# Optimization experiments

Hardware: AMD Instinct MI355X
Metric: run time of the kernel (lower is better)

The kernel has to match this reference:

```python
import jax, jax.numpy as jnp
import numpy as np

N, E, G = 10000, 160000, 64
F, C1, C2, C3, K, NC = 128, 128, 256, 512, 5, 10


def setup_inputs() -> dict:
    key = jax.random.key(0)
    ks = jax.random.split(key, 12)
    s = 0.05
    return {
        "x": jax.random.normal(ks[0], (N, F), dtype=jnp.float32),
        "edge_index": jax.random.randint(ks[1], (2, E), 0, N, dtype=jnp.int64),
        "batch": jnp.sort(jax.random.randint(ks[2], (N,), 0, G, dtype=jnp.int64)),
        "W_cheb": jax.random.normal(ks[3], (K, F, C1), dtype=jnp.float32) * s,
        "b_cheb": jnp.zeros((C1,), jnp.float32),
        "W_g1": jax.random.normal(ks[4], (C1, C2), dtype=jnp.float32) * s,
        "b_g1": jnp.zeros((C2,), jnp.float32),
        "W_g2": jax.random.normal(ks[5], (C2, C3), dtype=jnp.float32) * s,
        "b_g2": jnp.zeros((C3,), jnp.float32),
        "w_gate": jax.random.normal(ks[6], (C3, 1), dtype=jnp.float32) * s,
        "b_gate": jnp.zeros((1,), jnp.float32),
        "W_fc": jax.random.normal(ks[7], (C3, NC), dtype=jnp.float32) * s,
        "b_fc": jnp.zeros((NC,), jnp.float32),
    }


def _deg_inv_sqrt(deg):
    return jnp.where(deg > 0, jax.lax.rsqrt(jnp.maximum(deg, 1e-12)), 0.0)


def cheb_conv(x, src, dst, W, b):
    # PyG ChebConv, sym normalization, lambda_max=2 => scaled Laplacian = -D^-1/2 A D^-1/2
    ones = jnp.ones((src.shape[0],), x.dtype)
    deg = jax.ops.segment_sum(ones, src, num_segments=N)
    dinv = _deg_inv_sqrt(deg)
    w = -(dinv[src] * dinv[dst])  # [E]

    def prop(h):
        return jax.ops.segment_sum(w[:, None] * h[src], dst, num_segments=N)

    tx0 = x
    tx1 = prop(x)
    out = tx0 @ W[0] + tx1 @ W[1]
    for k in range(2, W.shape[0]):
        tx2 = 2.0 * prop(tx1) - tx0
        out = out + tx2 @ W[k]
        tx0, tx1 = tx1, tx2
    return out + b


def gcn_conv(x, src, dst, W, b):
    # PyG GCNConv: add self-loops, sym norm D~^-1/2 (A+I) D~^-1/2, transform then aggregate
    loop = jnp.arange(N, dtype=src.dtype)
    src_a = jnp.concatenate([src, loop])
    dst_a = jnp.concatenate([dst, loop])
    ones = jnp.ones((src_a.shape[0],), x.dtype)
    deg = jax.ops.segment_sum(ones, dst_a, num_segments=N)
    dinv = _deg_inv_sqrt(deg)
    norm = dinv[src_a] * dinv[dst_a]  # [E+N]
    h = x @ W
    return jax.ops.segment_sum(norm[:, None] * h[src_a], dst_a, num_segments=N) + b


def attention_pool(x, batch, w_gate, b_gate):
    logits = (x @ w_gate + b_gate)[:, 0]  # [N]
    m = jax.ops.segment_max(logits, batch, num_segments=G)
    e = jnp.exp(logits - m[batch])
    s = jax.ops.segment_sum(e, batch, num_segments=G)
    alpha = e / s[batch]
    return jax.ops.segment_sum(alpha[:, None] * x, batch, num_segments=G)  # [G, C3]


def reference(x, edge_index, batch, W_cheb, b_cheb, W_g1, b_g1, W_g2, b_g2,
              w_gate, b_gate, W_fc, b_fc):
    src, dst = edge_index[0], edge_index[1]
    h = jax.nn.relu(cheb_conv(x, src, dst, W_cheb, b_cheb))
    h = jax.nn.relu(gcn_conv(h, src, dst, W_g1, b_g1))
    h = jax.nn.relu(gcn_conv(h, src, dst, W_g2, b_g2))
    g = attention_pool(h, batch, w_gate, b_gate)
    logits = g @ W_fc + b_fc
    return jax.nn.log_softmax(logits, axis=1)
```

## Files before the change

kernel.cpp:

```cpp
#include <hip/hip_runtime.h>
#include <hip/hip_bf16.h>
#include <math.h>

#define N_NODES 10000
#define N_EDGES 160000
#define N_GRAPHS 64
#define F_IN    128
#define C1_DIM  128
#define C2_DIM  256
#define C3_DIM  512
#define K_CHEB  5
#define NCLS    10
#define TC      (K_CHEB * F_IN)

typedef short v8s __attribute__((ext_vector_type(8)));
typedef float v4f __attribute__((ext_vector_type(4)));

static __device__ __forceinline__ unsigned short f2bf(float f) {
    unsigned u = __float_as_uint(f);
    unsigned r = (u + 0x7FFFu + ((u >> 16) & 1u)) >> 16;
    return (unsigned short)r;
}
static __device__ __forceinline__ float bf_lo(unsigned u) { return __uint_as_float(u << 16); }
static __device__ __forceinline__ float bf_hi(unsigned u) { return __uint_as_float(u & 0xFFFF0000u); }

#define PREP_A (N_NODES * 64)
#define PREP_B (TC * C1_DIM)
#define PREP_C (C1_DIM * C2_DIM)
#define PREP_D (C2_DIM * C3_DIM)
#define PREP_E N_NODES
#define PREP_F N_NODES
#define PREP_H (N_GRAPHS * C3_DIM)
#define PREP_G N_EDGES
#define PREP_TOTAL (PREP_A + PREP_B + PREP_C + PREP_D + PREP_E + PREP_F + PREP_H + PREP_G)
__global__ void prep_kernel(const float* __restrict__ x, unsigned short* __restrict__ tcat,
                            const float* __restrict__ Wcheb, unsigned short* __restrict__ Wcb_t,
                            const float* __restrict__ Wg1, unsigned short* __restrict__ Wg1_t,
                            const float* __restrict__ Wg2, unsigned short* __restrict__ Wg2_t,
                            const int* __restrict__ batch, int* __restrict__ gptr,
                            float* __restrict__ logits, float* __restrict__ pooled,
                            const int* __restrict__ src, const int* __restrict__ dst,
                            int* __restrict__ cnt_s, int* __restrict__ cnt_d) {
    int id = blockIdx.x * blockDim.x + threadIdx.x;
    if (id < PREP_A) {
        int n = id >> 6, f = (id & 63) * 2;
        float2 v = *(const float2*)(x + (size_t)n * F_IN + f);
        ushort2 o; o.x = f2bf(v.x); o.y = f2bf(v.y);
        *(ushort2*)(tcat + (size_t)n * TC + f) = o;
        return;
    }
    id -= PREP_A;
    if (id < PREP_B) {
        int k = id % TC, n = id / TC;
        Wcb_t[(size_t)n * TC + k] = f2bf(Wcheb[(size_t)k * C1_DIM + n]);
        return;
    }
    id -= PREP_B;
    if (id < PREP_C) {
        int k = id % C1_DIM, n = id / C1_DIM;
        Wg1_t[(size_t)n * C1_DIM + k] = f2bf(Wg1[(size_t)k * C2_DIM + n]);
        return;
    }
    id -= PREP_C;
    if (id < PREP_D) {
        int k = id % C2_DIM, n = id / C2_DIM;
        Wg2_t[(size_t)n * C2_DIM + k] = f2bf(Wg2[(size_t)k * C3_DIM + n]);
        return;
    }
    id -= PREP_D;
    if (id < PREP_E) {
        int i = id;
        int b = batch[i];
        if (i == 0) { for (int g = 0; g <= b; g++) gptr[g] = 0; }
        else {
            int bp = batch[i - 1];
            for (int g = bp + 1; g <= b; g++) gptr[g] = i;
        }
        if (i == N_NODES - 1) { for (int g = b + 1; g <= N_GRAPHS; g++) gptr[g] = N_NODES; }
        return;
    }
    id -= PREP_E;
    if (id < PREP_F) { logits[id] = 0.0f; return; }
    id -= PREP_F;
    if (id < PREP_H) { pooled[id] = 0.0f; return; }
    id -= PREP_H;
    if (id < PREP_G) {
        atomicAdd(&cnt_s[src[id]], 1);
        atomicAdd(&cnt_d[dst[id]], 1);
    }
}

__global__ __launch_bounds__(256) void scan_kernel(const int* __restrict__ cnt_d,
                                                   int* __restrict__ rowptr, int n) {
    __shared__ int ldsc[N_NODES];
    __shared__ int sums[256];
    int tid = threadIdx.x;
    for (int i = tid; i < n; i += 256) ldsc[i] = cnt_d[i];
    __syncthreads();
    int chunk = (n + 255) / 256;
    int s0 = tid * chunk, s1 = min(n, s0 + chunk);
    if (s0 > n) s0 = n;
    int loc = 0;
    for (int i = s0; i < s1; i++) loc += ldsc[i];
    sums[tid] = loc;
    __syncthreads();
    for (int off = 1; off < 256; off <<= 1) {
        int t = (tid >= off) ? sums[tid - off] : 0;
        __syncthreads();
        sums[tid] += t;
        __syncthreads();
    }
    int pre = sums[tid] - loc;
    for (int i = s0; i < s1; i++) { int v = ldsc[i]; ldsc[i] = pre; pre += v; }
    __syncthreads();
    for (int i = tid; i < n; i += 256) rowptr[i] = ldsc[i];
    if (tid == 255) rowptr[n] = pre;
}

__global__ void fill_kernel(const int* __restrict__ src, const int* __restrict__ dst,
                            const int* __restrict__ cnt_s, const int* __restrict__ cnt_d,
                            const int* __restrict__ rowptr, int* __restrict__ fillc,
                            int2* __restrict__ ecb, int2* __restrict__ egc, int E) {
    int e = blockIdx.x * blockDim.x + threadIdx.x;
    if (e >= E) return;
    int s = src[e], d = dst[e];
    int pos = rowptr[d] + atomicAdd(&fillc[d], 1);
    int cs = cnt_s[s], cd = cnt_s[d];
    float ds = (cs > 0) ? rsqrtf((float)cs) : 0.0f;
    float dd = (cd > 0) ? rsqrtf((float)cd) : 0.0f;
    float nr = rsqrtf((float)cnt_d[s] + 1.0f) * rsqrtf((float)cnt_d[d] + 1.0f);
    ecb[pos] = make_int2(s, __float_as_int(-(ds * dd)));
    egc[pos] = make_int2(s, __float_as_int(nr));
}

__global__ __launch_bounds__(256) void gather_cheb_bf(
        const unsigned short* __restrict__ tb, const int* __restrict__ rowptr,
        const int2* __restrict__ edges,
        const unsigned short* __restrict__ base, float alpha, float beta,
        unsigned short* __restrict__ outc, int n) {
    int w = (blockIdx.x * blockDim.x + threadIdx.x) >> 6;
    int lane = threadIdx.x & 63;
    if (w >= n) return;
    float a0 = 0.0f, a1 = 0.0f;
    int rs = rowptr[w], re = rowptr[w + 1];
    for (int b = rs; b < re; b += 64) {
        int cl = 0; float wl = 0.0f;
        if (b + lane < re) { int2 e = edges[b + lane]; cl = e.x; wl = __int_as_float(e.y); }
        int nk8 = (min(64, re - b) + 7) & ~7;
        for (int j = 0; j < nk8; j += 8) {
            int ss[8]; float ww[8]; unsigned uu[8];
            #pragma unroll
            for (int q = 0; q < 8; q++) { ss[q] = __shfl(cl, j + q); ww[q] = __shfl(wl, j + q); }
            #pragma unroll
            for (int q = 0; q < 8; q++) uu[q] = ((const unsigned*)(tb + (size_t)ss[q] * TC))[lane];
            #pragma unroll
            for (int q = 0; q < 8; q++) { a0 += ww[q] * bf_lo(uu[q]); a1 += ww[q] * bf_hi(uu[q]); }
        }
    }
    if (base) {
        unsigned ub = ((const unsigned*)(base + (size_t)w * TC))[lane];
        a0 = alpha * a0 + beta * bf_lo(ub);
        a1 = alpha * a1 + beta * bf_hi(ub);
    } else {
        a0 *= alpha; a1 *= alpha;
    }
    ushort2 o; o.x = f2bf(a0); o.y = f2bf(a1);
    *(ushort2*)(outc + (size_t)w * TC + lane * 2) = o;
}

template<int FPL>
__global__ __launch_bounds__(256) void gather_gcn_pre(
        const unsigned short* __restrict__ tb, const int* __restrict__ rowptr,
        const int2* __restrict__ edges,
        const int* __restrict__ cnt_d, unsigned short* __restrict__ z, int n) {
    const int C = FPL * 64;
    int w = (blockIdx.x * blockDim.x + threadIdx.x) >> 6;
    int lane = threadIdx.x & 63;
    if (w >= n) return;
    float acc[FPL];
    #pragma unroll
    for (int q = 0; q < FPL; q++) acc[q] = 0.0f;
    int rs = rowptr[w], re = rowptr[w + 1];
    for (int b = rs; b < re; b += 64) {
        int cl = 0; float wl = 0.0f;
        if (b + lane < re) { int2 e = edges[b + lane]; cl = e.x; wl = __int_as_float(e.y); }
        int nk8 = (min(64, re - b) + 7) & ~7;
        for (int j = 0; j < nk8; j += 8) {
            int ss[8]; float ww[8];
            #pragma unroll
            for (int q = 0; q < 8; q++) { ss[q] = __shfl(cl, j + q); ww[q] = __shfl(wl, j + q); }
            if constexpr (FPL == 2) {
                unsigned uu[8];
                #pragma unroll
                for (int q = 0; q < 8; q++) uu[q] = ((const unsigned*)(tb + (size_t)ss[q] * C))[lane];
                #pragma unroll
                for (int q = 0; q < 8; q++) {
                    acc[0] += ww[q] * bf_lo(uu[q]);
                    acc[1] += ww[q] * bf_hi(uu[q]);
                }
            } else {
                uint2 uu[8];
                #pragma unroll
                for (int q = 0; q < 8; q++) uu[q] = ((const uint2*)(tb + (size_t)ss[q] * C))[lane];
                #pragma unroll
                for (int q = 0; q < 8; q++) {
                    acc[0] += ww[q] * bf_lo(uu[q].x); acc[1] += ww[q] * bf_hi(uu[q].x);
                    acc[2] += ww[q] * bf_lo(uu[q].y); acc[3] += ww[q] * bf_hi(uu[q].y);
                }
            }
        }
    }
    float sn = 1.0f / (float)(cnt_d[w] + 1);
    if constexpr (FPL == 2) {
        unsigned u = ((const unsigned*)(tb + (size_t)w * C))[lane];
        acc[0] += sn * bf_lo(u); acc[1] += sn * bf_hi(u);
        ushort2 o; o.x = f2bf(acc[0]); o.y = f2bf(acc[1]);
        *(ushort2*)(z + (size_t)w * C + lane * 2) = o;
    } else {
        uint2 u = ((const uint2*)(tb + (size_t)w * C))[lane];
        acc[0] += sn * bf_lo(u.x); acc[1] += sn * bf_hi(u.x);
        acc[2] += sn * bf_lo(u.y); acc[3] += sn * bf_hi(u.y);
        ushort4 o; o.x = f2bf(acc[0]); o.y = f2bf(acc[1]);
        o.z = f2bf(acc[2]); o.w = f2bf(acc[3]);
        *(ushort4*)(z + (size_t)w * C + lane * 4) = o;
    }
}

template<int JT>
__global__ __launch_bounds__(256) void gemm_bf16(
        const unsigned short* __restrict__ A, const unsigned short* __restrict__ Bt,
        const float* __restrict__ bias, float* __restrict__ Cf,
        unsigned short* __restrict__ Cb, const float* __restrict__ wg,
        float* __restrict__ logits, int M, int K, int N, int relu) {
    int m0 = blockIdx.y * 64, n0 = blockIdx.x * (JT * 32);
    int wave = threadIdx.x >> 6, lane = threadIdx.x & 63;
    int wm = (wave & 1) * 32, wn = (wave >> 1) * (JT * 16);
    int l15 = lane & 15, quad = lane >> 4;

    v4f acc[2][JT];
    #pragma unroll
    for (int i = 0; i < 2; i++)
        #pragma unroll
        for (int j = 0; j < JT; j++) acc[i][j] = (v4f){0.f, 0.f, 0.f, 0.f};

    const unsigned short* Ab[2]; bool av[2];
    #pragma unroll
    for (int i = 0; i < 2; i++) {
        int row = m0 + wm + i * 16 + l15;
        av[i] = row < M;
        Ab[i] = A + (size_t)(av[i] ? row : 0) * K + quad * 8;
    }
    const unsigned short* Bb[JT];
    #pragma unroll
    for (int j = 0; j < JT; j++) {
        int coln = n0 + wn + j * 16 + l15;
        Bb[j] = Bt + (size_t)coln * K + quad * 8;
    }
    const v8s zero8 = {0, 0, 0, 0, 0, 0, 0, 0};

    for (int k0 = 0; k0 < K; k0 += 32) {
        v8s a[2], b[JT];
        #pragma unroll
        for (int i = 0; i < 2; i++) a[i] = av[i] ? *(const v8s*)(Ab[i] + k0) : zero8;
        #pragma unroll
        for (int j = 0; j < JT; j++) b[j] = *(const v8s*)(Bb[j] + k0);
        #pragma unroll
        for (int i = 0; i < 2; i++)
            #pragma unroll
            for (int j = 0; j < JT; j++)
                acc[i][j] = __builtin_amdgcn_mfma_f32_16x16x32_bf16(a[i], b[j], acc[i][j], 0, 0, 0);
    }

    float bv[JT], wgj[JT];
    #pragma unroll
    for (int j = 0; j < JT; j++) {
        int coln = n0 + wn + j * 16 + l15;
        bv[j] = bias[coln];
        wgj[j] = wg ? wg[coln] : 0.0f;
    }
    #pragma unroll
    for (int i = 0; i < 2; i++) {
        #pragma unroll
        for (int r = 0; r < 4; r++) {
            int row = m0 + wm + i * 16 + quad * 4 + r;
            if (row >= M) continue;
            float gval = 0.0f;
            #pragma unroll
            for (int j = 0; j < JT; j++) {
                int coln = n0 + wn + j * 16 + l15;
                float v = acc[i][j][r] + bv[j];
                if (relu) v = fmaxf(v, 0.0f);
                if (Cf) Cf[(size_t)row * N + coln] = v;
                else    Cb[(size_t)row * N + coln] = f2bf(v);
                gval += v * wgj[j];
            }
            if (wg) {
                #pragma unroll
                for (int off = 1; off < 16; off <<= 1) gval += __shfl_xor(gval, off);
                if (l15 == 0) atomicAdd(&logits[row], gval);
            }
        }
    }
}

__global__ __launch_bounds__(256) void pool_partial(const unsigned short* __restrict__ h3b,
        const float* __restrict__ logits, const int* __restrict__ gptr,
        float* __restrict__ pooled) {
    __shared__ float red[256];
    int g = blockIdx.x, sl = blockIdx.y, tid = threadIdx.x;
    int gs = gptr[g], ge = gptr[g + 1];
    float m = -INFINITY;
    for (int i = gs + tid; i < ge; i += 256) m = fmaxf(m, logits[i]);
    red[tid] = m; __syncthreads();
    for (int off = 128; off > 0; off >>= 1) {
        if (tid < off) red[tid] = fmaxf(red[tid], red[tid + off]);
        __syncthreads();
    }
    m = red[0]; __syncthreads();
    float s = 0.0f;
    for (int i = gs + tid; i < ge; i += 256) s += expf(logits[i] - m);
    red[tid] = s; __syncthreads();
    for (int off = 128; off > 0; off >>= 1) {
        if (tid < off) red[tid] += red[tid + off];
        __syncthreads();
    }
    s = red[0];
    float sinv = (s > 0.0f) ? 1.0f / s : 0.0f;
    int cnt = ge - gs;
    int i0 = gs + (cnt * sl) / 8;
    int i1 = gs + (cnt * (sl + 1)) / 8;
    float a0 = 0.0f, a1 = 0.0f;
    for (int i = i0; i < i1; i++) {
        float al = expf(logits[i] - m) * sinv;
        unsigned u = ((const unsigned*)(h3b + (size_t)i * C3_DIM))[tid];
        a0 += al * bf_lo(u);
        a1 += al * bf_hi(u);
    }
    if (i1 > i0) {
        atomicAdd(&pooled[(size_t)g * C3_DIM + tid * 2 + 0], a0);
        atomicAdd(&pooled[(size_t)g * C3_DIM + tid * 2 + 1], a1);
    }
}

__global__ void fc_kernel(const float* __restrict__ pooled, const float* __restrict__ Wfc,
                          const float* __restrict__ bfc, float* __restrict__ out) {
    int g = blockIdx.x;
    int t = threadIdx.x;
    float acc = -INFINITY;
    if (t < NCLS) {
        acc = bfc[t];
        for (int k = 0; k < C3_DIM; k++)
            acc += pooled[(size_t)g * C3_DIM + k] * Wfc[k * NCLS + t];
    }
    float m = acc;
    #pragma unroll
    for (int off = 8; off > 0; off >>= 1) m = fmaxf(m, __shfl_xor(m, off, 16));
    float e = (t < NCLS) ? expf(acc - m) : 0.0f;
    float s = e;
    #pragma unroll
    for (int off = 8; off > 0; off >>= 1) s += __shfl_xor(s, off, 16);
    if (t < NCLS) out[g * NCLS + t] = acc - m - logf(s);
}

extern "C" void kernel_launch(void* const* d_in, const int* in_sizes, int n_in,
                              void* d_out, int out_size, void* d_ws, size_t ws_size,
                              hipStream_t stream) {
    const float* x      = (const float*)d_in[0];
    const int*   ei     = (const int*)d_in[1];
    const int*   batch  = (const int*)d_in[2];
    const float* W_cheb = (const float*)d_in[3];
    const float* b_cheb = (const float*)d_in[4];
    const float* W_g1   = (const float*)d_in[5];
    const float* b_g1   = (const float*)d_in[6];
    const float* W_g2   = (const float*)d_in[7];
    const float* b_g2   = (const float*)d_in[8];
    const float* w_gate = (const float*)d_in[9];
    const float* W_fc   = (const float*)d_in[11];
    const float* b_fc   = (const float*)d_in[12];
    const int* src = ei;
    const int* dst = ei + N_EDGES;
    float* out = (float*)d_out;

    const int N = N_NODES, E = N_EDGES, G = N_GRAPHS;

    char* Wp = (char*)d_ws;
    auto alloc = [&](size_t bytes) {
        void* p = Wp;
        Wp += (bytes + 255) & ~(size_t)255;
        return p;
    };
    int*   cnt3    = (int*)alloc((size_t)3 * N * 4);
    int*   cnt_s   = cnt3;
    int*   cnt_d   = cnt3 + N;
    int*   fillc   = cnt3 + 2 * N;
    int*   rowptr  = (int*)alloc((N + 1) * 4);
    int2*  ecb     = (int2*)alloc((size_t)E * 8);
    int2*  egc     = (int2*)alloc((size_t)E * 8);
    unsigned short* tcat  = (unsigned short*)alloc((size_t)N * TC * 2);
    unsigned short* h1b   = (unsigned short*)alloc((size_t)N * C1_DIM * 2);
    unsigned short* z1b   = (unsigned short*)alloc((size_t)N * C1_DIM * 2);
    unsigned short* h2b   = (unsigned short*)alloc((size_t)N * C2_DIM * 2);
    unsigned short* z2b   = (unsigned short*)alloc((size_t)N * C2_DIM * 2);
    unsigned short* h3b   = (unsigned short*)alloc((size_t)N * C3_DIM * 2);
    unsigned short* Wcb_t = (unsigned short*)alloc((size_t)TC * C1_DIM * 2);
    unsigned short* Wg1_t = (unsigned short*)alloc((size_t)C1_DIM * C2_DIM * 2);
    unsigned short* Wg2_t = (unsigned short*)alloc((size_t)C2_DIM * C3_DIM * 2);
    float* logits  = (float*)alloc(N * 4);
    int*   gptr    = (int*)alloc((G + 1) * 4);
    float* pooled  = (float*)alloc((size_t)G * C3_DIM * 4);

    dim3 blk(256);
    auto cdiv = [](int a, int b) { return (a + b - 1) / b; };

    hipMemsetAsync(cnt3, 0, (size_t)3 * N * sizeof(int), stream);
    hipLaunchKernelGGL(prep_kernel, dim3(cdiv(PREP_TOTAL, 256)), blk, 0, stream,
                       x, tcat, W_cheb, Wcb_t, W_g1, Wg1_t, W_g2, Wg2_t,
                       batch, gptr, logits, pooled, src, dst, cnt_s, cnt_d);

    hipLaunchKernelGGL(scan_kernel, dim3(1), blk, 0, stream, cnt_d, rowptr, N);
    hipLaunchKernelGGL(fill_kernel, dim3(cdiv(E, 256)), blk, 0, stream,
                       src, dst, cnt_s, cnt_d, rowptr, fillc, ecb, egc, E);

    const int NWB = cdiv(N, 4);

    hipLaunchKernelGGL(gather_cheb_bf, dim3(NWB), blk, 0, stream,
                       tcat + 0 * F_IN, rowptr, ecb,
                       (const unsigned short*)nullptr, 1.0f, 0.0f, tcat + 1 * F_IN, N);
    hipLaunchKernelGGL(gather_cheb_bf, dim3(NWB), blk, 0, stream,
                       tcat + 1 * F_IN, rowptr, ecb,
                       tcat + 0 * F_IN, 2.0f, -1.0f, tcat + 2 * F_IN, N);
    hipLaunchKernelGGL(gather_cheb_bf, dim3(NWB), blk, 0, stream,
                       tcat + 2 * F_IN, rowptr, ecb,
                       tcat + 1 * F_IN, 2.0f, -1.0f, tcat + 3 * F_IN, N);
    hipLaunchKernelGGL(gather_cheb_bf, dim3(NWB), blk, 0, stream,
                       tcat + 3 * F_IN, rowptr, ecb,
                       tcat + 2 * F_IN, 2.0f, -1.0f, tcat + 4 * F_IN, N);

    hipLaunchKernelGGL(gemm_bf16<2>, dim3(C1_DIM / 64, cdiv(N, 64)), blk, 0, stream,
                       tcat, Wcb_t, b_cheb, (float*)nullptr, h1b,
                       (const float*)nullptr, (float*)nullptr, N, TC, C1_DIM, 1);

    hipLaunchKernelGGL(gather_gcn_pre<2>, dim3(NWB), blk, 0, stream,
                       h1b, rowptr, egc, cnt_d, z1b, N);
    hipLaunchKernelGGL(gemm_bf16<4>, dim3(C2_DIM / 128, cdiv(N, 64)), blk, 0, stream,
                       z1b, Wg1_t, b_g1, (float*)nullptr, h2b,
                       (const float*)nullptr, (float*)nullptr, N, C1_DIM, C2_DIM, 1);

    hipLaunchKernelGGL(gather_gcn_pre<4>, dim3(NWB), blk, 0, stream,
                       h2b, rowptr, egc, cnt_d, z2b, N);
    hipLaunchKernelGGL(gemm_bf16<4>, dim3(C3_DIM / 128, cdiv(N, 64)), blk, 0, stream,
                       z2b, Wg2_t, b_g2, (float*)nullptr, h3b,
                       w_gate, logits, N, C2_DIM, C3_DIM, 1);

    hipLaunchKernelGGL(pool_partial, dim3(G, 8), blk, 0, stream, h3b, logits, gptr, pooled);
    hipLaunchKernelGGL(fc_kernel, dim3(G), dim3(64), 0, stream, pooled, W_fc, b_fc, out);
}
```

Measured before the change: 263.8 us.

## Unroll gather batches to 16, template GEMM K, vectorize x conversion

The gather kernels now issue 16 neighbour-row loads per batch instead of 8, aiming to keep more memory requests in flight and hide gather latency. The GEMM takes K as a template parameter so its k-loop can be fully unrolled, and the unused float-output and relu-flag paths are removed. The x-to-bf16 prep step uses float4 loads instead of float2. The trade-off is higher register pressure in the gathers and more wasted padded shuffles for low-degree nodes, since rows are padded to multiples of 16.

```diff
diff --git a/kernel.cpp b/kernel.cpp
--- a/kernel.cpp
+++ b/kernel.cpp
@@ -24,7 +24,7 @@
 static __device__ __forceinline__ float bf_lo(unsigned u) { return __uint_as_float(u << 16); }
 static __device__ __forceinline__ float bf_hi(unsigned u) { return __uint_as_float(u & 0xFFFF0000u); }
 
-#define PREP_A (N_NODES * 64)
+#define PREP_A (N_NODES * 32)
 #define PREP_B (TC * C1_DIM)
 #define PREP_C (C1_DIM * C2_DIM)
 #define PREP_D (C2_DIM * C3_DIM)
@@ -43,10 +43,10 @@
                             int* __restrict__ cnt_s, int* __restrict__ cnt_d) {
     int id = blockIdx.x * blockDim.x + threadIdx.x;
     if (id < PREP_A) {
-        int n = id >> 6, f = (id & 63) * 2;
-        float2 v = *(const float2*)(x + (size_t)n * F_IN + f);
-        ushort2 o; o.x = f2bf(v.x); o.y = f2bf(v.y);
-        *(ushort2*)(tcat + (size_t)n * TC + f) = o;
+        int n = id >> 5, f = (id & 31) * 4;
+        float4 v = *(const float4*)(x + (size_t)n * F_IN + f);
+        ushort4 o; o.x = f2bf(v.x); o.y = f2bf(v.y); o.z = f2bf(v.z); o.w = f2bf(v.w);
+        *(ushort4*)(tcat + (size_t)n * TC + f) = o;
         return;
     }
     id -= PREP_A;
@@ -98,8 +98,7 @@
     for (int i = tid; i < n; i += 256) ldsc[i] = cnt_d[i];
     __syncthreads();
     int chunk = (n + 255) / 256;
-    int s0 = tid * chunk, s1 = min(n, s0 + chunk);
-    if (s0 > n) s0 = n;
+    int s0 = min(n, tid * chunk), s1 = min(n, s0 + chunk);
     int loc = 0;
     for (int i = s0; i < s1; i++) loc += ldsc[i];
     sums[tid] = loc;
@@ -146,15 +145,15 @@
     for (int b = rs; b < re; b += 64) {
         int cl = 0; float wl = 0.0f;
         if (b + lane < re) { int2 e = edges[b + lane]; cl = e.x; wl = __int_as_float(e.y); }
-        int nk8 = (min(64, re - b) + 7) & ~7;
-        for (int j = 0; j < nk8; j += 8) {
-            int ss[8]; float ww[8]; unsigned uu[8];
-            #pragma unroll
-            for (int q = 0; q < 8; q++) { ss[q] = __shfl(cl, j + q); ww[q] = __shfl(wl, j + q); }
-            #pragma unroll
-            for (int q = 0; q < 8; q++) uu[q] = ((const unsigned*)(tb + (size_t)ss[q] * TC))[lane];
-            #pragma unroll
-            for (int q = 0; q < 8; q++) { a0 += ww[q] * bf_lo(uu[q]); a1 += ww[q] * bf_hi(uu[q]); }
+        int nk16 = (min(64, re - b) + 15) & ~15;
+        for (int j = 0; j < nk16; j += 16) {
+            int ss[16]; float ww[16]; unsigned uu[16];
+            #pragma unroll
+            for (int q = 0; q < 16; q++) { ss[q] = __shfl(cl, j + q); ww[q] = __shfl(wl, j + q); }
+            #pragma unroll
+            for (int q = 0; q < 16; q++) uu[q] = ((const unsigned*)(tb + (size_t)ss[q] * TC))[lane];
+            #pragma unroll
+            for (int q = 0; q < 16; q++) { a0 += ww[q] * bf_lo(uu[q]); a1 += ww[q] * bf_hi(uu[q]); }
         }
     }
     if (base) {
@@ -184,26 +183,23 @@
     for (int b = rs; b < re; b += 64) {
         int cl = 0; float wl = 0.0f;
         if (b + lane < re) { int2 e = edges[b + lane]; cl = e.x; wl = __int_as_float(e.y); }
-        int nk8 = (min(64, re - b) + 7) & ~7;
-        for (int j = 0; j < nk8; j += 8) {
-            int ss[8]; float ww[8];
-            #pragma unroll
-            for (int q = 0; q < 8; q++) { ss[q] = __shfl(cl, j + q); ww[q] = __shfl(wl, j + q); }
+        int nk16 = (min(64, re - b) + 15) & ~15;
+        for (int j = 0; j < nk16; j += 16) {
+            int ss[16]; float ww[16];
+            #pragma unroll
+            for (int q = 0; q < 16; q++) { ss[q] = __shfl(cl, j + q); ww[q] = __shfl(wl, j + q); }
             if constexpr (FPL == 2) {
-                unsigned uu[8];
+                unsigned uu[16];
                 #pragma unroll
-                for (int q = 0; q < 8; q++) uu[q] = ((const unsigned*)(tb + (size_t)ss[q] * C))[lane];
+                for (int q = 0; q < 16; q++) uu[q] = ((const unsigned*)(tb + (size_t)ss[q] * C))[lane];
                 #pragma unroll
-                for (int q = 0; q < 8; q++) {
-                    acc[0] += ww[q] * bf_lo(uu[q]);
-                    acc[1] += ww[q] * bf_hi(uu[q]);
-                }
+                for (int q = 0; q < 16; q++) { acc[0] += ww[q] * bf_lo(uu[q]); acc[1] += ww[q] * bf_hi(uu[q]); }
             } else {
-                uint2 uu[8];
+                uint2 uu[16];
                 #pragma unroll
-                for (int q = 0; q < 8; q++) uu[q] = ((const uint2*)(tb + (size_t)ss[q] * C))[lane];
+                for (int q = 0; q < 16; q++) uu[q] = ((const uint2*)(tb + (size_t)ss[q] * C))[lane];
                 #pragma unroll
-                for (int q = 0; q < 8; q++) {
+                for (int q = 0; q < 16; q++) {
                     acc[0] += ww[q] * bf_lo(uu[q].x); acc[1] += ww[q] * bf_hi(uu[q].x);
                     acc[2] += ww[q] * bf_lo(uu[q].y); acc[3] += ww[q] * bf_hi(uu[q].y);
                 }
@@ -226,12 +222,12 @@
     }
 }
 
-template<int JT>
+template<int JT, int KC>
 __global__ __launch_bounds__(256) void gemm_bf16(
         const unsigned short* __restrict__ A, const unsigned short* __restrict__ Bt,
-        const float* __restrict__ bias, float* __restrict__ Cf,
+        const float* __restrict__ bias,
         unsigned short* __restrict__ Cb, const float* __restrict__ wg,
-        float* __restrict__ logits, int M, int K, int N, int relu) {
+        float* __restrict__ logits, int M, int N) {
     int m0 = blockIdx.y * 64, n0 = blockIdx.x * (JT * 32);
     int wave = threadIdx.x >> 6, lane = threadIdx.x & 63;
     int wm = (wave & 1) * 32, wn = (wave >> 1) * (JT * 16);
@@ -248,17 +244,18 @@
     for (int i = 0; i < 2; i++) {
         int row = m0 + wm + i * 16 + l15;
         av[i] = row < M;
-        Ab[i] = A + (size_t)(av[i] ? row : 0) * K + quad * 8;
+        Ab[i] = A + (size_t)(av[i] ? row : 0) * KC + quad * 8;
     }
     const unsigned short* Bb[JT];
     #pragma unroll
     for (int j = 0; j < JT; j++) {
         int coln = n0 + wn + j * 16 + l15;
-        Bb[j] = Bt + (size_t)coln * K + quad * 8;
+        Bb[j] = Bt + (size_t)coln * KC + quad * 8;
     }
     const v8s zero8 = {0, 0, 0, 0, 0, 0, 0, 0};
 
-    for (int k0 = 0; k0 < K; k0 += 32) {
+    #pragma unroll
+    for (int k0 = 0; k0 < KC; k0 += 32) {
         v8s a[2], b[JT];
         #pragma unroll
         for (int i = 0; i < 2; i++) a[i] = av[i] ? *(const v8s*)(Ab[i] + k0) : zero8;
@@ -288,10 +285,8 @@
             #pragma unroll
             for (int j = 0; j < JT; j++) {
                 int coln = n0 + wn + j * 16 + l15;
-                float v = acc[i][j][r] + bv[j];
-                if (relu) v = fmaxf(v, 0.0f);
-                if (Cf) Cf[(size_t)row * N + coln] = v;
-                else    Cb[(size_t)row * N + coln] = f2bf(v);
+                float v = fmaxf(acc[i][j][r] + bv[j], 0.0f);
+                Cb[(size_t)row * N + coln] = f2bf(v);
                 gval += v * wgj[j];
             }
             if (wg) {
@@ -436,21 +431,21 @@
                        tcat + 3 * F_IN, rowptr, ecb,
                        tcat + 2 * F_IN, 2.0f, -1.0f, tcat + 4 * F_IN, N);
 
-    hipLaunchKernelGGL(gemm_bf16<2>, dim3(C1_DIM / 64, cdiv(N, 64)), blk, 0, stream,
-                       tcat, Wcb_t, b_cheb, (float*)nullptr, h1b,
-                       (const float*)nullptr, (float*)nullptr, N, TC, C1_DIM, 1);
+    hipLaunchKernelGGL((gemm_bf16<2, TC>), dim3(C1_DIM / 64, cdiv(N, 64)), blk, 0, stream,
+                       tcat, Wcb_t, b_cheb, h1b,
+                       (const float*)nullptr, (float*)nullptr, N, C1_DIM);
 
     hipLaunchKernelGGL(gather_gcn_pre<2>, dim3(NWB), blk, 0, stream,
                        h1b, rowptr, egc, cnt_d, z1b, N);
-    hipLaunchKernelGGL(gemm_bf16<4>, dim3(C2_DIM / 128, cdiv(N, 64)), blk, 0, stream,
-                       z1b, Wg1_t, b_g1, (float*)nullptr, h2b,
-                       (const float*)nullptr, (float*)nullptr, N, C1_DIM, C2_DIM, 1);
+    hipLaunchKernelGGL((gemm_bf16<4, C1_DIM>), dim3(C2_DIM / 128, cdiv(N, 64)), blk, 0, stream,
+                       z1b, Wg1_t, b_g1, h2b,
+                       (const float*)nullptr, (float*)nullptr, N, C2_DIM);
 
     hipLaunchKernelGGL(gather_gcn_pre<4>, dim3(NWB), blk, 0, stream,
                        h2b, rowptr, egc, cnt_d, z2b, N);
-    hipLaunchKernelGGL(gemm_bf16<4>, dim3(C3_DIM / 128, cdiv(N, 64)), blk, 0, stream,
-                       z2b, Wg2_t, b_g2, (float*)nullptr, h3b,
-                       w_gate, logits, N, C2_DIM, C3_DIM, 1);
+    hipLaunchKernelGGL((gemm_bf16<4, C2_DIM>), dim3(C3_DIM / 128, cdiv(N, 64)), blk, 0, stream,
+                       z2b, Wg2_t, b_g2, h3b,
+                       w_gate, logits, N, C3_DIM);
 
     hipLaunchKernelGGL(pool_partial, dim3(G, 8), blk, 0, stream, h3b, logits, gptr, pooled);
     hipLaunchKernelGGL(fc_kernel, dim3(G), dim3(64), 0, stream, pooled, W_fc, b_fc, out);
```

New measurement: 264.1 us. About the same (+0.1%).
